# Kernel tuning notes

Measured on AMD Instinct MI355X. Metric: run time of the kernel, lower is better.

## Reference

```python
import jax, jax.numpy as jnp
import numpy as np

B, S, D, H = 2, 2048, 2048, 16
HD = D // H  # head_dim = 128


def setup_inputs() -> dict:
    key = jax.random.key(0)
    ks = jax.random.split(key, 9)
    s = 1.0 / np.sqrt(D)
    return {
        "x": jax.random.normal(ks[0], (B, S, D), jnp.float32),
        "Wq": jax.random.normal(ks[1], (D, D), jnp.float32) * s,
        "bq": jax.random.normal(ks[2], (D,), jnp.float32) * 0.02,
        "Wk": jax.random.normal(ks[3], (D, D), jnp.float32) * s,
        "bk": jax.random.normal(ks[4], (D,), jnp.float32) * 0.02,
        "Wv": jax.random.normal(ks[5], (D, D), jnp.float32) * s,
        "bv": jax.random.normal(ks[6], (D,), jnp.float32) * 0.02,
        "Wo": jax.random.normal(ks[7], (D, D), jnp.float32) * s,
        "bo": jax.random.normal(ks[8], (D,), jnp.float32) * 0.02,
    }


def reference(x, Wq, bq, Wk, bk, Wv, bv, Wo, bo):
    b, s, d = x.shape
    # nn.Linear: y = x @ W.T + b
    def split(t):
        # [b, s, d] -> [b, H, s, HD]
        return t.reshape(b, s, H, HD).transpose(0, 2, 1, 3)

    q = split(x @ Wq.T + bq)
    k = split(x @ Wk.T + bk)
    v = split(x @ Wv.T + bv)

    scale = jnp.asarray(HD, x.dtype) ** 0.5
    qk = jnp.einsum("bhqd,bhkd->bhqk", q, k) / scale  # [b, H, s, s]
    weights = jax.nn.softmax(qk, axis=-1)
    attn = jnp.einsum("bhqk,bhkd->bhqd", weights, v)  # [b, H, s, HD]

    merged = attn.transpose(0, 2, 1, 3).reshape(b, s, d)
    return merged @ Wo.T + bo
```

## Files before the change

kernel.cpp:

```cpp
#include <hip/hip_runtime.h>

typedef __bf16 bf16_t;
typedef bf16_t bf16x8 __attribute__((ext_vector_type(8)));
typedef bf16_t bf16x4 __attribute__((ext_vector_type(4)));
typedef float  f32x4  __attribute__((ext_vector_type(4)));

#define DDIM  2048
#define SEQ   2048
#define NH    16
#define HDIM  128
#define BATCH 2
#define MROWS (BATCH * SEQ)
#define XEL   ((size_t)MROWS * DDIM)
#define WEL   ((size_t)DDIM * DDIM)

__device__ __forceinline__ void async_ld16(const bf16_t* g, bf16_t* l) {
  __builtin_amdgcn_global_load_lds(
      (const __attribute__((address_space(1))) void*)g,
      (__attribute__((address_space(3))) void*)l, 16, 0, 0);
}

__global__ void cvt_all(const float* __restrict__ x,
                        const float* __restrict__ w0,
                        const float* __restrict__ w1,
                        const float* __restrict__ w2,
                        const float* __restrict__ w3,
                        bf16_t* __restrict__ ox, bf16_t* __restrict__ ow) {
  const size_t CX = XEL / 4;
  const size_t CW = WEL / 4;
  const size_t total = CX + 4 * CW;
  size_t c = (size_t)blockIdx.x * blockDim.x + threadIdx.x;
  const size_t stride = (size_t)gridDim.x * blockDim.x;
  for (; c < total; c += stride) {
    float4 v;
    bf16_t* outp;
    if (c < CX) {
      v = reinterpret_cast<const float4*>(x)[c];
      outp = ox + c * 4;
    } else {
      const size_t d = c - CX;
      const size_t seg = d >> 20;
      const float* w = seg == 0 ? w0 : seg == 1 ? w1 : seg == 2 ? w2 : w3;
      v = reinterpret_cast<const float4*>(w)[d & (CW - 1)];
      outp = ow + d * 4;
    }
    bf16x4 o;
    o[0] = (bf16_t)v.x; o[1] = (bf16_t)v.y;
    o[2] = (bf16_t)v.z; o[3] = (bf16_t)v.w;
    *reinterpret_cast<bf16x4*>(outp) = o;
  }
}

#define LGKM(N)                                                               \
  asm volatile("s_waitcnt lgkmcnt(" #N ")" ::: "memory");                     \
  __builtin_amdgcn_sched_barrier(0);

__global__ __launch_bounds__(512, 2) void gemm_qkv(
    const bf16_t* __restrict__ Ax, const bf16_t* __restrict__ Wcat,
    const float* __restrict__ bq, const float* __restrict__ bk,
    const float* __restrict__ bv,
    bf16_t* __restrict__ QKVh, float qscale) {
  __shared__ __align__(16) bf16_t smem[57344];

  const int tid  = threadIdx.x;
  const int lane = tid & 63;
  const int w    = tid >> 6;
  const int wm   = w >> 2;
  const int wn   = w & 3;
  const int lg   = lane >> 4;
  const int lr   = lane & 15;

  const int bid = blockIdx.x;
  const int l   = (bid & 7) * 64 + (bid >> 3);
  const int tm  = l & 15;
  const int tn  = l >> 4;
  const int row0  = tm * 256;
  const int ncol0 = tn * 192;

  auto SA  = [&](int buf, int ha) { return smem + (buf * 2 + ha) * 8192; };
  auto SBp = [&](int buf) { return smem + 32768 + buf * 12288; };

  auto stA = [&](int buf, int ha, int kt) {
#pragma unroll
    for (int L = 0; L < 2; ++L) {
      const int c = L * 512 + tid, r = c >> 3, ch = c & 7;
      async_ld16(Ax + (size_t)(row0 + ha * 128 + r) * DDIM + kt * 64 +
                     ((ch ^ (r & 7)) * 8),
                 SA(buf, ha) + c * 8);
    }
  };
  auto stB = [&](int buf, int kt) {
#pragma unroll
    for (int L = 0; L < 3; ++L) {
      const int c = L * 512 + tid, r = c >> 3, ch = c & 7;
      async_ld16(Wcat + (size_t)(ncol0 + r) * DDIM + kt * 64 +
                     ((ch ^ (r & 7)) * 8),
                 SBp(buf) + c * 8);
    }
  };
  auto ldA = [&](int buf, int mf, int k) {
    const int row = mf * 16 + lr;
    const int ch  = (k * 4 + lg) ^ (row & 7);
    return *reinterpret_cast<const bf16x8*>(SA(buf, wm) + row * 64 + ch * 8);
  };
  auto ldB = [&](int buf, int nf, int k) {
    const int row = wn * 48 + nf * 16 + lr;
    const int ch  = (k * 4 + lg) ^ (row & 7);
    return *reinterpret_cast<const bf16x8*>(SBp(buf) + row * 64 + ch * 8);
  };

  f32x4  acc[8][3] = {};
  bf16x8 a[8][2];
  bf16x8 bfr[3][2];

#define MFMA_PH(Q)                                                            \
  __builtin_amdgcn_s_setprio(1);                                              \
  _Pragma("unroll") for (int k = 0; k < 2; ++k) {                             \
    _Pragma("unroll") for (int nf = 0; nf < 3; ++nf) {                        \
      acc[2 * (Q)][nf] = __builtin_amdgcn_mfma_f32_16x16x32_bf16(             \
          a[2 * (Q)][k], bfr[nf][k], acc[2 * (Q)][nf], 0, 0, 0);              \
      acc[2 * (Q) + 1][nf] = __builtin_amdgcn_mfma_f32_16x16x32_bf16(         \
          a[2 * (Q) + 1][k], bfr[nf][k], acc[2 * (Q) + 1][nf], 0, 0, 0);      \
    }                                                                         \
  }                                                                           \
  __builtin_amdgcn_s_setprio(0);

#define HALF(BUF, ST1, ST2)                                                   \
  {                                                                           \
       \
    a[0][0] = ldA(BUF, 0, 0); a[0][1] = ldA(BUF, 0, 1);                       \
    a[1][0] = ldA(BUF, 1, 0); a[1][1] = ldA(BUF, 1, 1);                       \
    _Pragma("unroll") for (int nf = 0; nf < 3; ++nf) {                        \
      bfr[nf][0] = ldB(BUF, nf, 0); bfr[nf][1] = ldB(BUF, nf, 1);             \
    }                                                                         \
    __builtin_amdgcn_sched_barrier(0);                                        \
    a[2][0] = ldA(BUF, 2, 0); a[2][1] = ldA(BUF, 2, 1);                       \
    a[3][0] = ldA(BUF, 3, 0); a[3][1] = ldA(BUF, 3, 1);                       \
    __builtin_amdgcn_sched_barrier(0);                                        \
    a[4][0] = ldA(BUF, 4, 0); a[4][1] = ldA(BUF, 4, 1);                       \
    a[5][0] = ldA(BUF, 5, 0); a[5][1] = ldA(BUF, 5, 1);                       \
    __builtin_amdgcn_sched_barrier(0);                                        \
    a[6][0] = ldA(BUF, 6, 0); a[6][1] = ldA(BUF, 6, 1);                       \
    a[7][0] = ldA(BUF, 7, 0); a[7][1] = ldA(BUF, 7, 1);                       \
    ST1;                                                                      \
    asm volatile("s_waitcnt lgkmcnt(12)" ::: "memory");                       \
    __builtin_amdgcn_sched_barrier(0);                                        \
    __builtin_amdgcn_s_barrier();                                             \
    MFMA_PH(0)                                                                \
    ST2;                                                                      \
    asm volatile("s_waitcnt lgkmcnt(8)" ::: "memory");                        \
    __builtin_amdgcn_sched_barrier(0);                                        \
    MFMA_PH(1)                                                                \
    asm volatile("s_waitcnt lgkmcnt(4)" ::: "memory");                        \
    __builtin_amdgcn_sched_barrier(0);                                        \
    MFMA_PH(2)                                                                \
    asm volatile("s_waitcnt lgkmcnt(0)" ::: "memory");                        \
    __builtin_amdgcn_sched_barrier(0);                                        \
    MFMA_PH(3)                                                                \
    asm volatile("s_waitcnt vmcnt(3)" ::: "memory");                          \
    __builtin_amdgcn_s_barrier();                                             \
  }

  stA(0, 0, 0); stA(0, 1, 0);
  stB(0, 0);
  stB(1, 1);
  asm volatile("s_waitcnt vmcnt(3)" ::: "memory");
  __builtin_amdgcn_s_barrier();

  for (int i = 0; i < 16; ++i) {
    const int t1 = (2 * i + 1) & 31;
    const int t2 = (2 * i + 2) & 31;
    const int t3 = (2 * i + 3) & 31;
    HALF(0, { stA(1, 0, t1); stA(1, 1, t1); }, { stB(0, t2); })
    HALF(1, { stA(0, 0, t2); stA(0, 1, t2); }, { stB(1, t3); })
  }
#undef HALF
#undef MFMA_PH
  asm volatile("s_waitcnt vmcnt(0)" ::: "memory");
  __builtin_amdgcn_s_barrier();

  const int bblk = row0 >> 11;
  const int s0b  = row0 & (SEQ - 1);
#pragma unroll
  for (int mf = 0; mf < 8; ++mf) {
    const int rr0 = row0 + wm * 128 + mf * 16 + lg * 4;
    const int s0 = rr0 & (SEQ - 1);
#pragma unroll
    for (int nf = 0; nf < 3; ++nf) {
      const int col = ncol0 + wn * 48 + nf * 16 + lr;
      const int mat = col >> 11;
      const int c2  = col & (DDIM - 1);
      const float bs = ((mat == 0) ? bq : (mat == 1) ? bk : bv)[c2];
      if (mat == 2) {
        const int lc = wn * 48 + nf * 16 + lr;
        const int ls = wm * 128 + mf * 16 + lg * 4;
        bf16x4 pk;
#pragma unroll
        for (int r = 0; r < 4; ++r) pk[r] = (bf16_t)(acc[mf][nf][r] + bs);
        *reinterpret_cast<bf16x4*>(&smem[lc * 264 + ls]) = pk;
      } else {
        const float scl = (mat == 0) ? qscale : 1.0f;
        const int h = c2 >> 7, hd = c2 & (HDIM - 1);
        bf16_t* outb = QKVh + (size_t)mat * XEL;
#pragma unroll
        for (int r = 0; r < 4; ++r) {
          outb[(((size_t)(bblk * NH + h)) * SEQ + s0 + r) * HDIM + hd] =
              (bf16_t)((acc[mf][nf][r] + bs) * scl);
        }
      }
    }
  }

  const int vstart = (ncol0 >= 4096) ? 0
                   : ((4096 - ncol0) < 192 ? (4096 - ncol0) : 192);
  const int vcnt = 192 - vstart;
  if (vcnt > 0) {
    asm volatile("s_waitcnt lgkmcnt(0)" ::: "memory");
    __builtin_amdgcn_s_barrier();
    bf16_t* outV = QKVh + (size_t)2 * XEL;
    const int nchunk = vcnt * 32;
    for (int cc = tid; cc < nchunk; cc += 512) {
      const int lc = vstart + (cc >> 5);
      const int sc = (cc & 31) * 8;
      bf16x8 v = *reinterpret_cast<const bf16x8*>(&smem[lc * 264 + sc]);
      const int c2 = ncol0 + lc - 4096;
      const int h = c2 >> 7, hd = c2 & (HDIM - 1);
      *reinterpret_cast<bf16x8*>(
          &outV[(((size_t)(bblk * NH + h)) * HDIM + hd) * SEQ + s0b + sc]) = v;
    }
  }
}

#define QMM(NF, BV)                                                           \
  __builtin_amdgcn_s_setprio(1);                                              \
  _Pragma("unroll") for (int mf = 0; mf < 4; ++mf) {                          \
    acc[mf][NF] = __builtin_amdgcn_mfma_f32_16x16x32_bf16(                    \
        a_[mf][0], BV[0], acc[mf][NF], 0, 0, 0);                              \
    acc[mf][NF] = __builtin_amdgcn_mfma_f32_16x16x32_bf16(                    \
        a_[mf][1], BV[1], acc[mf][NF], 0, 0, 0);                              \
  }                                                                           \
  __builtin_amdgcn_s_setprio(0);

__global__ __launch_bounds__(512, 2) void gemm_bt(
    const bf16_t* __restrict__ A, const bf16_t* __restrict__ Bw,
    const float* __restrict__ bias, float* __restrict__ outp) {
  __shared__ __align__(16) bf16_t sA[2][2][128 * 64];
  __shared__ __align__(16) bf16_t sB[3][128 * 64];

  const int tid  = threadIdx.x;
  const int lane = tid & 63;
  const int w    = tid >> 6;
  const int wm   = w >> 1;
  const int wn   = w & 1;
  const int lg   = lane >> 4;
  const int lr   = lane & 15;

  const int bid = blockIdx.x;
  const int l   = (bid & 7) * 32 + (bid >> 3);
  const int tm  = l & 15;
  const int tn  = l >> 4;
  const int row0 = tm * 256;
  const int col0 = tn * 128;

  auto stA = [&](int buf, int ha, int kt) {
#pragma unroll
    for (int L = 0; L < 2; ++L) {
      const int c = L * 512 + tid, r = c >> 3, ch = c & 7;
      async_ld16(A + (size_t)(row0 + ha * 128 + r) * DDIM + kt * 64 +
                     ((ch ^ (r & 7)) * 8),
                 &sA[buf][ha][c * 8]);
    }
  };
  auto stB = [&](int buf, int kt) {
#pragma unroll
    for (int L = 0; L < 2; ++L) {
      const int c = L * 512 + tid, r = c >> 3, ch = c & 7;
      async_ld16(Bw + (size_t)(col0 + r) * DDIM + kt * 64 +
                     ((ch ^ (r & 7)) * 8),
                 &sB[buf][c * 8]);
    }
  };
  auto ldA = [&](int buf, int mf, int k) {
    const int row = (wm & 1) * 64 + mf * 16 + lr;
    const int ch  = (k * 4 + lg) ^ (row & 7);
    return *reinterpret_cast<const bf16x8*>(
        &sA[buf][wm >> 1][row * 64 + ch * 8]);
  };
  auto ldB = [&](int buf, int nf, int k) {
    const int row = wn * 64 + nf * 16 + lr;
    const int ch  = (k * 4 + lg) ^ (row & 7);
    return *reinterpret_cast<const bf16x8*>(&sB[buf][row * 64 + ch * 8]);
  };

  f32x4 acc[4][4] = {};

  stA(0, 0, 0); stA(0, 1, 0);
  stB(0, 0);
  stB(1, 1);
  asm volatile("s_waitcnt vmcnt(2)" ::: "memory");
  __builtin_amdgcn_s_barrier();

  int bc = 0;
  for (int t = 0; t < 32; ++t) {
    const int p   = t & 1;
    const int pn  = p ^ 1;
    const int tn1 = (t + 1) & 31, tn2 = (t + 2) & 31;
    const int b2i = bc == 0 ? 2 : bc - 1;

    bf16x8 a_[4][2];
#pragma unroll
    for (int mf = 0; mf < 4; ++mf) {
      a_[mf][0] = ldA(p, mf, 0);
      a_[mf][1] = ldA(p, mf, 1);
    }
    bf16x8 b0[2], b1[2], b2[2], b3[2];
    b0[0] = ldB(bc, 0, 0); b0[1] = ldB(bc, 0, 1);
    b1[0] = ldB(bc, 1, 0); b1[1] = ldB(bc, 1, 1);
    b2[0] = ldB(bc, 2, 0); b2[1] = ldB(bc, 2, 1);
    __builtin_amdgcn_sched_barrier(0);
    stA(pn, 0, tn1); stA(pn, 1, tn1);
    stB(b2i, tn2);
    __builtin_amdgcn_sched_barrier(0);
    LGKM(4)
    QMM(0, b0)
    b3[0] = ldB(bc, 3, 0); b3[1] = ldB(bc, 3, 1);
    __builtin_amdgcn_sched_barrier(0);
    LGKM(4)
    QMM(1, b1)
    LGKM(2)
    QMM(2, b2)
    LGKM(0)
    QMM(3, b3)
    asm volatile("s_waitcnt vmcnt(2)" ::: "memory");
    __builtin_amdgcn_s_barrier();
    bc = bc == 2 ? 0 : bc + 1;
  }
  asm volatile("s_waitcnt vmcnt(0)" ::: "memory");

#pragma unroll
  for (int mf = 0; mf < 4; ++mf) {
    const int row = row0 + wm * 64 + mf * 16 + lg * 4;
#pragma unroll
    for (int nf = 0; nf < 4; ++nf) {
      const int col = col0 + wn * 64 + nf * 16 + lr;
      const float bs = bias[col];
#pragma unroll
      for (int r = 0; r < 4; ++r)
        outp[(size_t)(row + r) * DDIM + col] = acc[mf][nf][r] + bs;
    }
  }
}

__global__ __launch_bounds__(256) void attn_fwd(
    const bf16_t* __restrict__ Q, const bf16_t* __restrict__ K,
    const bf16_t* __restrict__ Vt, bf16_t* __restrict__ out) {
  __shared__ __align__(16) bf16_t sK[64 * 128];
  __shared__ __align__(16) bf16_t sV[128 * 64];
  __shared__ __align__(16) bf16_t sP[4][32][72];

  const int tid  = threadIdx.x;
  const int lane = tid & 63;
  const int w    = tid >> 6;
  const int lg   = lane >> 4;
  const int lr   = lane & 15;

  const int bid     = blockIdx.x;
  const int logical = (bid & 7) * 64 + (bid >> 3);
  const int bh      = logical >> 4;
  const int q0      = (logical & 15) * 128;
  const int qw      = q0 + w * 32;

  const bf16_t* Kb = K  + (size_t)bh * SEQ * HDIM;
  const bf16_t* Vb = Vt + (size_t)bh * HDIM * SEQ;

  bf16x8 qf[2][4];
#pragma unroll
  for (int mf = 0; mf < 2; ++mf) {
    const bf16_t* qbase = Q + ((size_t)bh * SEQ + qw + mf * 16 + lr) * HDIM;
#pragma unroll
    for (int kc = 0; kc < 4; ++kc)
      qf[mf][kc] = *reinterpret_cast<const bf16x8*>(qbase + kc * 32 + lg * 8);
  }

  bf16x8 onesf;
#pragma unroll
  for (int i = 0; i < 8; ++i) onesf[i] = (bf16_t)1.0f;

  f32x4 o[2][8] = {};
  f32x4 o1[2] = {};

  for (int kv0 = 0; kv0 < SEQ; kv0 += 64) {
    __syncthreads();
#pragma unroll
    for (int p = 0; p < 4; ++p) {
      const int slot = p * 256 + tid;
      const int kr = slot >> 4, kc = slot & 15;
      async_ld16(Kb + ((size_t)(kv0 + kr)) * HDIM + ((kc ^ (kr & 7)) * 8),
                 sK + slot * 8);
      const int vr = slot >> 3, vc = slot & 7;
      async_ld16(Vb + (size_t)vr * SEQ + kv0 + ((vc ^ (vr & 7)) * 8),
                 sV + slot * 8);
    }
    __syncthreads();

    f32x4 s[2][4] = {};
    __builtin_amdgcn_s_setprio(1);
#pragma unroll
    for (int kc = 0; kc < 4; ++kc) {
#pragma unroll
      for (int cb = 0; cb < 4; ++cb) {
        const int r  = cb * 16 + lr;
        const int ch = kc * 4 + lg;
        bf16x8 kf = *reinterpret_cast<const bf16x8*>(
            sK + r * 128 + ((ch ^ (r & 7)) * 8));
        s[0][cb] = __builtin_amdgcn_mfma_f32_16x16x32_bf16(qf[0][kc], kf, s[0][cb], 0, 0, 0);
        s[1][cb] = __builtin_amdgcn_mfma_f32_16x16x32_bf16(qf[1][kc], kf, s[1][cb], 0, 0, 0);
      }
    }
    __builtin_amdgcn_s_setprio(0);

#pragma unroll
    for (int mf = 0; mf < 2; ++mf)
#pragma unroll
      for (int r = 0; r < 4; ++r)
#pragma unroll
        for (int cb = 0; cb < 4; ++cb) {
          const float p = __builtin_amdgcn_exp2f(s[mf][cb][r]);
          sP[w][mf * 16 + lg * 4 + r][cb * 16 + lr] = (bf16_t)p;
        }

    asm volatile("s_waitcnt lgkmcnt(0)" ::: "memory");

    __builtin_amdgcn_s_setprio(1);
#pragma unroll
    for (int ks = 0; ks < 2; ++ks) {
      bf16x8 pf0 = *reinterpret_cast<const bf16x8*>(&sP[w][lr][ks * 32 + lg * 8]);
      bf16x8 pf1 = *reinterpret_cast<const bf16x8*>(&sP[w][16 + lr][ks * 32 + lg * 8]);
      o1[0] = __builtin_amdgcn_mfma_f32_16x16x32_bf16(pf0, onesf, o1[0], 0, 0, 0);
      o1[1] = __builtin_amdgcn_mfma_f32_16x16x32_bf16(pf1, onesf, o1[1], 0, 0, 0);
#pragma unroll
      for (int ob = 0; ob < 8; ++ob) {
        const int r  = ob * 16 + lr;
        const int ch = ks * 4 + lg;
        bf16x8 vf = *reinterpret_cast<const bf16x8*>(
            sV + r * 64 + ((ch ^ (r & 7)) * 8));
        o[0][ob] = __builtin_amdgcn_mfma_f32_16x16x32_bf16(pf0, vf, o[0][ob], 0, 0, 0);
        o[1][ob] = __builtin_amdgcn_mfma_f32_16x16x32_bf16(pf1, vf, o[1][ob], 0, 0, 0);
      }
    }
    __builtin_amdgcn_s_setprio(0);
  }

  const int b = bh >> 4, h = bh & 15;
#pragma unroll
  for (int mf = 0; mf < 2; ++mf) {
#pragma unroll
    for (int r = 0; r < 4; ++r) {
      const float inv_l = 1.0f / o1[mf][r];
      const int row = qw + mf * 16 + lg * 4 + r;
      bf16_t* obase = out + ((size_t)b * SEQ + row) * DDIM + h * HDIM;
#pragma unroll
      for (int ob = 0; ob < 8; ++ob)
        obase[ob * 16 + lr] = (bf16_t)(o[mf][ob][r] * inv_l);
    }
  }
}

extern "C" void kernel_launch(void* const* d_in, const int* in_sizes, int n_in,
                              void* d_out, int out_size, void* d_ws,
                              size_t ws_size, hipStream_t stream) {
  const float* x  = (const float*)d_in[0];
  const float* Wq = (const float*)d_in[1];
  const float* bq = (const float*)d_in[2];
  const float* Wk = (const float*)d_in[3];
  const float* bk = (const float*)d_in[4];
  const float* Wv = (const float*)d_in[5];
  const float* bv = (const float*)d_in[6];
  const float* Wo = (const float*)d_in[7];
  const float* bo = (const float*)d_in[8];

  bf16_t* ws = (bf16_t*)d_ws;
  const size_t XE = XEL;
  const size_t WE = WEL;
  bf16_t* xb  = ws;
  bf16_t* wqb = ws + XE;
  bf16_t* wkb = wqb + WE;
  bf16_t* wvb = wkb + WE;
  bf16_t* wob = wvb + WE;
  bf16_t* Qh  = wob + WE;
  bf16_t* Kh  = Qh + XE;
  bf16_t* Vt  = Kh + XE;
  bf16_t* merged = xb;

  cvt_all<<<2048, 256, 0, stream>>>(x, Wq, Wk, Wv, Wo, xb, wqb);

  const float qscale = 0.12751744520778695f;

  gemm_qkv<<<512, 512, 0, stream>>>(xb, wqb, bq, bk, bv, Qh, qscale);

  attn_fwd<<<512, 256, 0, stream>>>(Qh, Kh, Vt, merged);

  gemm_bt<<<256, 512, 0, stream>>>(merged, wob, bo, (float*)d_out);
}
```

Before: 246.1 us.

## Single-buffer QKV GEMM LDS to raise occupancy, split V transpose epilogue

```diff
diff --git a/kernel.cpp b/kernel.cpp
--- a/kernel.cpp
+++ b/kernel.cpp
@@ -55,12 +55,12 @@
   asm volatile("s_waitcnt lgkmcnt(" #N ")" ::: "memory");                     \
   __builtin_amdgcn_sched_barrier(0);
 
-__global__ __launch_bounds__(512, 2) void gemm_qkv(
+__global__ __launch_bounds__(512, 4) void gemm_qkv(
     const bf16_t* __restrict__ Ax, const bf16_t* __restrict__ Wcat,
     const float* __restrict__ bq, const float* __restrict__ bk,
     const float* __restrict__ bv,
     bf16_t* __restrict__ QKVh, float qscale) {
-  __shared__ __align__(16) bf16_t smem[57344];
+  __shared__ __align__(16) bf16_t smem[28672];
 
   const int tid  = threadIdx.x;
   const int lane = tid & 63;
@@ -77,36 +77,36 @@
   const int row0  = tm * 256;
   const int ncol0 = tn * 192;
 
-  auto SA  = [&](int buf, int ha) { return smem + (buf * 2 + ha) * 8192; };
-  auto SBp = [&](int buf) { return smem + 32768 + buf * 12288; };
-
-  auto stA = [&](int buf, int ha, int kt) {
+  auto SA = [&](int ha) { return smem + ha * 8192; };
+  bf16_t* SB = smem + 16384;
+
+  auto stA = [&](int ha, int kt) {
 #pragma unroll
     for (int L = 0; L < 2; ++L) {
       const int c = L * 512 + tid, r = c >> 3, ch = c & 7;
       async_ld16(Ax + (size_t)(row0 + ha * 128 + r) * DDIM + kt * 64 +
                      ((ch ^ (r & 7)) * 8),
-                 SA(buf, ha) + c * 8);
-    }
-  };
-  auto stB = [&](int buf, int kt) {
+                 SA(ha) + c * 8);
+    }
+  };
+  auto stB = [&](int kt) {
 #pragma unroll
     for (int L = 0; L < 3; ++L) {
       const int c = L * 512 + tid, r = c >> 3, ch = c & 7;
       async_ld16(Wcat + (size_t)(ncol0 + r) * DDIM + kt * 64 +
                      ((ch ^ (r & 7)) * 8),
-                 SBp(buf) + c * 8);
-    }
-  };
-  auto ldA = [&](int buf, int mf, int k) {
+                 SB + c * 8);
+    }
+  };
+  auto ldA = [&](int mf, int k) {
     const int row = mf * 16 + lr;
     const int ch  = (k * 4 + lg) ^ (row & 7);
-    return *reinterpret_cast<const bf16x8*>(SA(buf, wm) + row * 64 + ch * 8);
-  };
-  auto ldB = [&](int buf, int nf, int k) {
+    return *reinterpret_cast<const bf16x8*>(SA(wm) + row * 64 + ch * 8);
+  };
+  auto ldB = [&](int nf, int k) {
     const int row = wn * 48 + nf * 16 + lr;
     const int ch  = (k * 4 + lg) ^ (row & 7);
-    return *reinterpret_cast<const bf16x8*>(SBp(buf) + row * 64 + ch * 8);
+    return *reinterpret_cast<const bf16x8*>(SB + row * 64 + ch * 8);
   };
 
   f32x4  acc[8][3] = {};
@@ -125,59 +125,46 @@
   }                                                                           \
   __builtin_amdgcn_s_setprio(0);
 
-#define HALF(BUF, ST1, ST2)                                                   \
-  {                                                                           \
-       \
-    a[0][0] = ldA(BUF, 0, 0); a[0][1] = ldA(BUF, 0, 1);                       \
-    a[1][0] = ldA(BUF, 1, 0); a[1][1] = ldA(BUF, 1, 1);                       \
-    _Pragma("unroll") for (int nf = 0; nf < 3; ++nf) {                        \
-      bfr[nf][0] = ldB(BUF, nf, 0); bfr[nf][1] = ldB(BUF, nf, 1);             \
-    }                                                                         \
-    __builtin_amdgcn_sched_barrier(0);                                        \
-    a[2][0] = ldA(BUF, 2, 0); a[2][1] = ldA(BUF, 2, 1);                       \
-    a[3][0] = ldA(BUF, 3, 0); a[3][1] = ldA(BUF, 3, 1);                       \
-    __builtin_amdgcn_sched_barrier(0);                                        \
-    a[4][0] = ldA(BUF, 4, 0); a[4][1] = ldA(BUF, 4, 1);                       \
-    a[5][0] = ldA(BUF, 5, 0); a[5][1] = ldA(BUF, 5, 1);                       \
-    __builtin_amdgcn_sched_barrier(0);                                        \
-    a[6][0] = ldA(BUF, 6, 0); a[6][1] = ldA(BUF, 6, 1);                       \
-    a[7][0] = ldA(BUF, 7, 0); a[7][1] = ldA(BUF, 7, 1);                       \
-    ST1;                                                                      \
-    asm volatile("s_waitcnt lgkmcnt(12)" ::: "memory");                       \
-    __builtin_amdgcn_sched_barrier(0);                                        \
-    __builtin_amdgcn_s_barrier();                                             \
-    MFMA_PH(0)                                                                \
-    ST2;                                                                      \
-    asm volatile("s_waitcnt lgkmcnt(8)" ::: "memory");                        \
-    __builtin_amdgcn_sched_barrier(0);                                        \
-    MFMA_PH(1)                                                                \
-    asm volatile("s_waitcnt lgkmcnt(4)" ::: "memory");                        \
-    __builtin_amdgcn_sched_barrier(0);                                        \
-    MFMA_PH(2)                                                                \
-    asm volatile("s_waitcnt lgkmcnt(0)" ::: "memory");                        \
-    __builtin_amdgcn_sched_barrier(0);                                        \
-    MFMA_PH(3)                                                                \
-    asm volatile("s_waitcnt vmcnt(3)" ::: "memory");                          \
-    __builtin_amdgcn_s_barrier();                                             \
-  }
-
-  stA(0, 0, 0); stA(0, 1, 0);
-  stB(0, 0);
-  stB(1, 1);
-  asm volatile("s_waitcnt vmcnt(3)" ::: "memory");
-  __builtin_amdgcn_s_barrier();
-
-  for (int i = 0; i < 16; ++i) {
-    const int t1 = (2 * i + 1) & 31;
-    const int t2 = (2 * i + 2) & 31;
-    const int t3 = (2 * i + 3) & 31;
-    HALF(0, { stA(1, 0, t1); stA(1, 1, t1); }, { stB(0, t2); })
-    HALF(1, { stA(0, 0, t2); stA(0, 1, t2); }, { stB(1, t3); })
-  }
-#undef HALF
-#undef MFMA_PH
+  stA(0, 0); stA(1, 0);
+  stB(0);
   asm volatile("s_waitcnt vmcnt(0)" ::: "memory");
   __builtin_amdgcn_s_barrier();
+
+  for (int t = 0; t < 32; ++t) {
+    const int tn1 = (t + 1) & 31;
+
+    a[0][0] = ldA(0, 0); a[0][1] = ldA(0, 1);
+    a[1][0] = ldA(1, 0); a[1][1] = ldA(1, 1);
+#pragma unroll
+    for (int nf = 0; nf < 3; ++nf) {
+      bfr[nf][0] = ldB(nf, 0); bfr[nf][1] = ldB(nf, 1);
+    }
+    __builtin_amdgcn_sched_barrier(0);
+    a[2][0] = ldA(2, 0); a[2][1] = ldA(2, 1);
+    a[3][0] = ldA(3, 0); a[3][1] = ldA(3, 1);
+    __builtin_amdgcn_sched_barrier(0);
+    a[4][0] = ldA(4, 0); a[4][1] = ldA(4, 1);
+    a[5][0] = ldA(5, 0); a[5][1] = ldA(5, 1);
+    __builtin_amdgcn_sched_barrier(0);
+    a[6][0] = ldA(6, 0); a[6][1] = ldA(6, 1);
+    a[7][0] = ldA(7, 0); a[7][1] = ldA(7, 1);
+    LGKM(12)
+    __builtin_amdgcn_s_barrier();
+    MFMA_PH(0)
+    LGKM(8)
+    MFMA_PH(1)
+    LGKM(4)
+    MFMA_PH(2)
+    LGKM(0)
+    __builtin_amdgcn_s_barrier();
+    stA(0, tn1); stA(1, tn1);
+    stB(tn1);
+    __builtin_amdgcn_sched_barrier(0);
+    MFMA_PH(3)
+    asm volatile("s_waitcnt vmcnt(0)" ::: "memory");
+    __builtin_amdgcn_s_barrier();
+  }
+#undef MFMA_PH
 
   const int bblk = row0 >> 11;
   const int s0b  = row0 & (SEQ - 1);
@@ -190,15 +177,8 @@
       const int col = ncol0 + wn * 48 + nf * 16 + lr;
       const int mat = col >> 11;
       const int c2  = col & (DDIM - 1);
-      const float bs = ((mat == 0) ? bq : (mat == 1) ? bk : bv)[c2];
-      if (mat == 2) {
-        const int lc = wn * 48 + nf * 16 + lr;
-        const int ls = wm * 128 + mf * 16 + lg * 4;
-        bf16x4 pk;
-#pragma unroll
-        for (int r = 0; r < 4; ++r) pk[r] = (bf16_t)(acc[mf][nf][r] + bs);
-        *reinterpret_cast<bf16x4*>(&smem[lc * 264 + ls]) = pk;
-      } else {
+      if (mat != 2) {
+        const float bs = ((mat == 0) ? bq : bk)[c2];
         const float scl = (mat == 0) ? qscale : 1.0f;
         const int h = c2 >> 7, hd = c2 & (HDIM - 1);
         bf16_t* outb = QKVh + (size_t)mat * XEL;
@@ -210,23 +190,44 @@
       }
     }
   }
-
-  const int vstart = (ncol0 >= 4096) ? 0
-                   : ((4096 - ncol0) < 192 ? (4096 - ncol0) : 192);
-  const int vcnt = 192 - vstart;
-  if (vcnt > 0) {
-    asm volatile("s_waitcnt lgkmcnt(0)" ::: "memory");
-    __builtin_amdgcn_s_barrier();
-    bf16_t* outV = QKVh + (size_t)2 * XEL;
-    const int nchunk = vcnt * 32;
-    for (int cc = tid; cc < nchunk; cc += 512) {
-      const int lc = vstart + (cc >> 5);
-      const int sc = (cc & 31) * 8;
-      bf16x8 v = *reinterpret_cast<const bf16x8*>(&smem[lc * 264 + sc]);
-      const int c2 = ncol0 + lc - 4096;
-      const int h = c2 >> 7, hd = c2 & (HDIM - 1);
-      *reinterpret_cast<bf16x8*>(
-          &outV[(((size_t)(bblk * NH + h)) * HDIM + hd) * SEQ + s0b + sc]) = v;
+  bf16_t* outV = QKVh + (size_t)2 * XEL;
+  for (int pass = 0; pass < 2; ++pass) {
+    __syncthreads();
+    if ((wn >> 1) == pass) {
+#pragma unroll
+      for (int mf = 0; mf < 8; ++mf) {
+        const int ls = wm * 128 + mf * 16 + lg * 4;
+#pragma unroll
+        for (int nf = 0; nf < 3; ++nf) {
+          const int col = ncol0 + wn * 48 + nf * 16 + lr;
+          if ((col >> 11) == 2) {
+            const int c2 = col & (DDIM - 1);
+            const float bs = bv[c2];
+            const int lc = (wn & 1) * 48 + nf * 16 + lr;
+            bf16x4 pk;
+#pragma unroll
+            for (int r = 0; r < 4; ++r) pk[r] = (bf16_t)(acc[mf][nf][r] + bs);
+            *reinterpret_cast<bf16x4*>(&smem[lc * 264 + ls]) = pk;
+          }
+        }
+      }
+    }
+    __syncthreads();
+    const int base = 96 * pass;
+    const int over = 4096 - ncol0 - base;
+    const int vs = over <= 0 ? 0 : (over >= 96 ? 96 : over);
+    const int vc = 96 - vs;
+    if (vc > 0) {
+      const int nchunk = vc * 32;
+      for (int cc = tid; cc < nchunk; cc += 512) {
+        const int lcw = vs + (cc >> 5);
+        const int sc = (cc & 31) * 8;
+        bf16x8 v = *reinterpret_cast<const bf16x8*>(&smem[lcw * 264 + sc]);
+        const int c2 = ncol0 + base + lcw - 4096;
+        const int h = c2 >> 7, hd = c2 & (HDIM - 1);
+        *reinterpret_cast<bf16x8*>(
+            &outV[(((size_t)(bblk * NH + h)) * HDIM + hd) * SEQ + s0b + sc]) = v;
+      }
     }
   }
 }
```

Measured after the change: 968.4 us. +293.6%, slower.
